# Kernel tuning notes

Hardware: AMD Instinct MI355X
Metric: run time of the kernel (lower is better)

The kernel has to match this reference:

```python
import jax, jax.numpy as jnp
import numpy as np

B, N, C = 16, 576, 1024
H, HD = 16, 64          # num_heads, head_dim
LMAX = 1024             # KV cache capacity
CUR = 256               # pre-existing cur_kv_len
HID = 4096              # mlp hidden
PREFIX = 64             # fixed prefix length from source
EPS = 1e-5


def _ln(x, w, b):
    m = x.mean(-1, keepdims=True)
    v = ((x - m) ** 2).mean(-1, keepdims=True)
    return (x - m) * jax.lax.rsqrt(v + EPS) * w + b


def setup_inputs() -> dict:
    key = jax.random.key(0)
    ks = jax.random.split(key, 8)
    s = 0.02
    return {
        "x": jax.random.normal(ks[0], (B, N, C), jnp.float32),
        "cache_k": jax.random.normal(ks[1], (B, H, LMAX, HD), jnp.float32),
        "cache_v": jax.random.normal(ks[2], (B, H, LMAX, HD), jnp.float32),
        "qkv_w": jax.random.normal(ks[3], (C, 3 * C), jnp.float32) * s,
        "qkv_b": jnp.zeros((3 * C,), jnp.float32),
        "proj_w": jax.random.normal(ks[4], (C, C), jnp.float32) * s,
        "proj_b": jnp.zeros((C,), jnp.float32),
        "norm1_w": jnp.ones((C,), jnp.float32),
        "norm1_b": jnp.zeros((C,), jnp.float32),
        "norm2_w": jnp.ones((C,), jnp.float32),
        "norm2_b": jnp.zeros((C,), jnp.float32),
        "fc1_w": jax.random.normal(ks[5], (C, HID), jnp.float32) * s,
        "fc1_b": jnp.zeros((HID,), jnp.float32),
        "fc2_w": jax.random.normal(ks[6], (HID, C), jnp.float32) * s,
        "fc2_b": jnp.zeros((C,), jnp.float32),
        "cur_kv_len": CUR,
    }


def reference(x, cache_k, cache_v, qkv_w, qkv_b, proj_w, proj_b,
              norm1_w, norm1_b, norm2_w, norm2_b,
              fc1_w, fc1_b, fc2_w, fc2_b, cur_kv_len):
    b, n, c = x.shape
    hd = c // H
    scale = hd ** -0.5

    # ---- attention branch (lazy_mar, not force-fresh) ----
    h = _ln(x, norm1_w, norm1_b)
    qkv = (h @ qkv_w + qkv_b).reshape(b, n, 3, H, hd).transpose(2, 0, 3, 1, 4)
    q, k, v = qkv[0], qkv[1], qkv[2]          # [B,H,N,hd]

    L = cur_kv_len                            # python int -> static slices
    app = n - PREFIX
    # scatter new keys/values into the cache: prefix at [0:64], lazy region appended
    ck = cache_k.at[:, :, PREFIX + L:PREFIX + L + app, :].set(k[:, :, PREFIX:, :])
    ck = ck.at[:, :, :PREFIX, :].set(k[:, :, :PREFIX, :])
    cv = cache_v.at[:, :, PREFIX + L:PREFIX + L + app, :].set(v[:, :, PREFIX:, :])
    cv = cv.at[:, :, :PREFIX, :].set(v[:, :, :PREFIX, :])

    avail = L + n                             # (L + app) + 64
    attn = jax.nn.softmax(
        jnp.einsum('bhqd,bhkd->bhqk', q * scale, ck[:, :, :avail, :]), axis=-1)
    o = jnp.einsum('bhqk,bhkd->bhqd', attn, cv[:, :, :avail, :])
    o = o.transpose(0, 2, 1, 3).reshape(b, n, c)
    x = x + (o @ proj_w + proj_b)

    # ---- MLP branch ----
    h2 = _ln(x, norm2_w, norm2_b)
    mlp = jax.nn.gelu(h2 @ fc1_w + fc1_b, approximate=False) @ fc2_w + fc2_b
    return x + mlp
```

## Files before the change

### kernel.cpp

```cpp
#include <hip/hip_runtime.h>

#define Bb 16
#define Nn_ 576
#define Cc 1024
#define Hh 16
#define HD 64
#define HID 4096
#define AVAIL 832
#define ROWS (Bb*Nn_)

typedef __bf16 bf16x8 __attribute__((ext_vector_type(8)));
typedef float f32x4 __attribute__((ext_vector_type(4)));

__device__ __forceinline__ unsigned short f2bf(float f) {
  unsigned u = __float_as_uint(f);
  u += 0x7FFF + ((u >> 16) & 1);
  return (unsigned short)(u >> 16);
}

__device__ __forceinline__ void glds16(const void* g, void* l) {
  __builtin_amdgcn_global_load_lds(
      (const __attribute__((address_space(1))) void*)g,
      (__attribute__((address_space(3))) void*)l, 16, 0, 0);
}

__device__ __forceinline__ bf16x8 ds_read128(const void* p) {
  bf16x8 r;
  asm volatile("ds_read_b128 %0, %1"
               : "=v"(r)
               : "v"((const __attribute__((address_space(3))) char*)p));
  return r;
}

#define BARR() asm volatile("s_barrier" ::: "memory")
#define VMCNT4() asm volatile("s_waitcnt vmcnt(4)" ::: "memory")
#define VMCNT0() asm volatile("s_waitcnt vmcnt(0)" ::: "memory")
#define LGKM0() asm volatile("s_waitcnt lgkmcnt(0)" ::: "memory")
#define LGKM8() asm volatile("s_waitcnt lgkmcnt(8)" ::: "memory")
#define SCHEDB() __builtin_amdgcn_sched_barrier(0)

__global__ void wtrans_k(const float* __restrict__ in, unsigned short* __restrict__ out,
                         int K, int N) {
  __shared__ float tile[32][33];
  int k0 = blockIdx.x * 32, n0 = blockIdx.y * 32;
  int tx = threadIdx.x, ty = threadIdx.y;
#pragma unroll
  for (int i = 0; i < 4; i++)
    tile[ty + i * 8][tx] = in[(size_t)(k0 + ty + i * 8) * N + n0 + tx];
  __syncthreads();
#pragma unroll
  for (int i = 0; i < 4; i++)
    out[(size_t)(n0 + ty + i * 8) * K + k0 + tx] = f2bf(tile[tx][ty + i * 8]);
}

__global__ void ln_k(const float* __restrict__ x, const float* __restrict__ w,
                     const float* __restrict__ bi, unsigned short* __restrict__ out) {
  int row = blockIdx.x;
  int t = threadIdx.x;
  float4 v = ((const float4*)(x + (size_t)row * Cc))[t];
  float s = v.x + v.y + v.z + v.w;
  float s2 = v.x * v.x + v.y * v.y + v.z * v.z + v.w * v.w;
#pragma unroll
  for (int off = 1; off < 64; off <<= 1) { s += __shfl_xor(s, off); s2 += __shfl_xor(s2, off); }
  __shared__ float red[8];
  int wid = t >> 6, lane = t & 63;
  if (lane == 0) { red[wid] = s; red[4 + wid] = s2; }
  __syncthreads();
  s = red[0] + red[1] + red[2] + red[3];
  s2 = red[4] + red[5] + red[6] + red[7];
  float mean = s * (1.0f / Cc);
  float var = s2 * (1.0f / Cc) - mean * mean;
  float rstd = rsqrtf(var + 1e-5f);
  float4 wv = ((const float4*)w)[t];
  float4 bv = ((const float4*)bi)[t];
  ushort4 ov;
  ov.x = f2bf((v.x - mean) * rstd * wv.x + bv.x);
  ov.y = f2bf((v.y - mean) * rstd * wv.y + bv.y);
  ov.z = f2bf((v.z - mean) * rstd * wv.z + bv.z);
  ov.w = f2bf((v.w - mean) * rstd * wv.w + bv.w);
  *(ushort4*)(out + (size_t)row * Cc + t * 4) = ov;
}

template <int EPI>
__global__ __launch_bounds__(512, 2) void gemm8_k(
    const unsigned short* __restrict__ A, const unsigned short* __restrict__ Bt,
    const float* __restrict__ bias, const float* __restrict__ resid,
    void* __restrict__ outv, int N, int K) {
  extern __shared__ __align__(16) char smem[];
  char* A0buf = smem;
  char* B0buf = smem + 32768;
  char* A1buf = smem + 65536;
  char* B1buf = smem + 98304;

  const int tid = threadIdx.x, lane = tid & 63, wid = tid >> 6;
  const int wr = wid >> 2, wc = wid & 3;
  const int l15 = lane & 15, l4 = lane >> 4;

  const int nwg = gridDim.x * gridDim.y;
  const int bid = blockIdx.y * gridDim.x + blockIdx.x;
  const int swz = (bid & 7) * (nwg >> 3) + (bid >> 3);
  const int m0 = (swz % gridDim.x) * 256, n0 = (swz / gridDim.x) * 256;

  const int KT = K >> 6;
  const size_t K2 = (size_t)K * 2;

  const int toff = (tid >> 3) * (int)K2 + ((((tid & 7) ^ ((tid >> 3) & 7)) << 4));
  const char* As0 = (const char*)A + (size_t)m0 * K2 + toff;
  const char* As1 = As0 + 128 * K2;
  const char* Bs0 = (const char*)Bt + (size_t)n0 * K2 + toff;
  const char* Bs1 = Bs0 + 128 * K2;
  const size_t l64 = 64 * K2;
  const int dst = tid * 16;

  const int s0 = ((l4 ^ (l15 & 7)) << 4);
  const int rbA = (wr * 128 + l15) * 128;
  const int rbB = (wc * 64 + l15) * 128;

  f32x4 acc[2][2][4][2] = {};
  bf16x8 a0[4][2], a1[4][2], bb0[2][2], bb1[2][2];

#define STAGE(srcH, ktb, ldsT, half)                        \
  do {                                                      \
    const char* _g = (srcH) + (size_t)(ktb);                \
    glds16(_g, (ldsT) + (half) * 16384 + dst);              \
    glds16(_g + l64, (ldsT) + (half) * 16384 + 8192 + dst); \
  } while (0)

#define RD_A(dA, CA, mh)                                                           \
  _Pragma("unroll") for (int mi = 0; mi < 4; ++mi)                                 \
  _Pragma("unroll") for (int ks = 0; ks < 2; ++ks)                                 \
    dA[mi][ks] = ds_read128((CA) + rbA + (mh) * 8192 + mi * 2048 + (s0 ^ (ks << 6)));

#define RD_B(dB, CB, nh)                                                           \
  _Pragma("unroll") for (int ni = 0; ni < 2; ++ni)                                 \
  _Pragma("unroll") for (int ks = 0; ks < 2; ++ks)                                 \
    dB[ni][ks] = ds_read128((CB) + rbB + (nh) * 4096 + ni * 2048 + (s0 ^ (ks << 6)));

#define MF(mh, nh, av, bv)                                                         \
  _Pragma("unroll") for (int mi = 0; mi < 4; ++mi)                                 \
  _Pragma("unroll") for (int ni = 0; ni < 2; ++ni)                                 \
  _Pragma("unroll") for (int ks = 0; ks < 2; ++ks)                                 \
    acc[mh][nh][mi][ni] = __builtin_amdgcn_mfma_f32_16x16x32_bf16(                 \
        av[mi][ks], bv[ni][ks], acc[mh][nh][mi][ni], 0, 0, 0);

#define TILE(CA, CB, OA, OB, t)                                       \
  do {                                                                \
    const size_t kt1 = (size_t)((t) + 1) * 128;                       \
    const size_t kt2 = (size_t)((t) + 2) * 128;                       \
                         \
    RD_A(a0, CA, 0); RD_B(bb0, CB, 0);                                \
    STAGE(Bs1, kt1, OB, 1);                                           \
    LGKM8();                                                          \
    BARR(); LGKM0(); SCHEDB();                                        \
    __builtin_amdgcn_s_setprio(1); MF(0, 0, a0, bb0);                 \
    __builtin_amdgcn_s_setprio(0); BARR();                            \
                         \
    RD_B(bb1, CB, 1);                                                 \
    STAGE(As1, kt1, OA, 1);                                           \
    BARR(); LGKM0(); SCHEDB();                                        \
    __builtin_amdgcn_s_setprio(1); MF(0, 1, a0, bb1);                 \
    __builtin_amdgcn_s_setprio(0); BARR();                            \
     \
    RD_A(a1, CA, 1);                                                  \
    STAGE(Bs0, kt2, CB, 0);                                           \
    BARR(); LGKM0(); SCHEDB();                                        \
    __builtin_amdgcn_s_setprio(1); MF(1, 0, a1, bb0);                 \
    __builtin_amdgcn_s_setprio(0); BARR();                            \
         \
    STAGE(As0, kt2, CA, 0);                                           \
    VMCNT4(); BARR();                                                 \
    __builtin_amdgcn_s_setprio(1); MF(1, 1, a1, bb1);                 \
    __builtin_amdgcn_s_setprio(0); BARR();                            \
  } while (0)

#define TILE_T1(CA, CB, OA, OB, t)                                    \
  do {                                                                \
    const size_t kt1 = (size_t)((t) + 1) * 128;                       \
    RD_A(a0, CA, 0); RD_B(bb0, CB, 0);                                \
    STAGE(Bs1, kt1, OB, 1);                                           \
    LGKM8();                                                          \
    BARR(); LGKM0(); SCHEDB();                                        \
    __builtin_amdgcn_s_setprio(1); MF(0, 0, a0, bb0);                 \
    __builtin_amdgcn_s_setprio(0); BARR();                            \
    RD_B(bb1, CB, 1);                                                 \
    STAGE(As1, kt1, OA, 1);                                           \
    BARR(); LGKM0(); SCHEDB();                                        \
    __builtin_amdgcn_s_setprio(1); MF(0, 1, a0, bb1);                 \
    __builtin_amdgcn_s_setprio(0); BARR();                            \
    RD_A(a1, CA, 1);                                                  \
    BARR(); LGKM0(); SCHEDB();                                        \
    __builtin_amdgcn_s_setprio(1); MF(1, 0, a1, bb0);                 \
    __builtin_amdgcn_s_setprio(0); BARR();                            \
    VMCNT0(); BARR();                                                 \
    __builtin_amdgcn_s_setprio(1); MF(1, 1, a1, bb1);                 \
    __builtin_amdgcn_s_setprio(0); BARR();                            \
  } while (0)

#define TILE_T2(CA, CB)                                               \
  do {                                                                \
    RD_A(a0, CA, 0); RD_B(bb0, CB, 0);                                \
    RD_B(bb1, CB, 1); RD_A(a1, CA, 1);                                \
    LGKM0(); SCHEDB();                                                \
    MF(0, 0, a0, bb0); MF(0, 1, a0, bb1);                             \
    MF(1, 0, a1, bb0); MF(1, 1, a1, bb1);                             \
  } while (0)

  STAGE(As0, 0, A0buf, 0);
  STAGE(Bs0, 0, B0buf, 0);
  STAGE(As1, 0, A0buf, 1);
  STAGE(Bs1, 0, B0buf, 1);
  STAGE(Bs0, 128, B1buf, 0);
  STAGE(As0, 128, A1buf, 0);
  VMCNT4();
  BARR();

#pragma unroll 1
  for (int t = 0; t + 3 < KT; t += 2) {
    TILE(A0buf, B0buf, A1buf, B1buf, t);
    TILE(A1buf, B1buf, A0buf, B0buf, t + 1);
  }
  TILE_T1(A0buf, B0buf, A1buf, B1buf, KT - 2);
  TILE_T2(A1buf, B1buf);

  BARR();
  {
    float* eb = (float*)(smem + wid * 16384);
    const int gc0 = n0 + wc * 64;
    const f32x4 bv4 = *(const f32x4*)&bias[gc0 + l15 * 4];
#pragma unroll
    for (int mh = 0; mh < 2; mh++) {
#pragma unroll
      for (int mi = 0; mi < 4; mi++) {
#pragma unroll
        for (int nh = 0; nh < 2; nh++)
#pragma unroll
          for (int ni = 0; ni < 2; ni++)
#pragma unroll
            for (int j = 0; j < 4; j++)
              eb[(l4 * 4 + j) * 68 + nh * 32 + ni * 16 + l15] = acc[mh][nh][mi][ni][j];
        int gr0 = m0 + wr * 128 + mh * 64 + mi * 16;
#pragma unroll
        for (int k = 0; k < 4; k++) {
          int r = k * 4 + l4;
          f32x4 v = *(const f32x4*)&eb[r * 68 + l15 * 4];
          v += bv4;
          size_t base = (size_t)(gr0 + r) * N + gc0 + l15 * 4;
          if (EPI == 1) {
#pragma unroll
            for (int q = 0; q < 4; q++)
              v[q] = 0.5f * v[q] * (1.0f + erff(v[q] * 0.70710678118f));
          }
          if (EPI == 2) {
            f32x4 rv = *(const f32x4*)&resid[base];
            *(f32x4*)((float*)outv + base) = v + rv;
          } else {
            ushort4 o4;
            o4.x = f2bf(v[0]); o4.y = f2bf(v[1]); o4.z = f2bf(v[2]); o4.w = f2bf(v[3]);
            *(ushort4*)((unsigned short*)outv + base) = o4;
          }
        }
      }
    }
  }
#undef TILE_T2
#undef TILE_T1
#undef TILE
#undef MF
#undef RD_B
#undef RD_A
#undef STAGE
}

__global__ void gatherk_k(const unsigned short* __restrict__ qkv,
                          const float* __restrict__ cache_k,
                          unsigned short* __restrict__ Kg) {
  int bh = blockIdx.y, b = bh >> 4, h = bh & 15;
  int p = blockIdx.x * 4 + (threadIdx.x >> 6);
  int d = threadIdx.x & 63;
  unsigned short val;
  if (p < 64)
    val = qkv[((size_t)(b * Nn_ + p)) * 3072 + 1024 + h * 64 + d];
  else if (p < 320)
    val = f2bf(cache_k[(((size_t)b * Hh + h) * 1024 + p) * 64 + d]);
  else
    val = qkv[((size_t)(b * Nn_ + p - 256)) * 3072 + 1024 + h * 64 + d];
  Kg[(((size_t)bh) * AVAIL + p) * 64 + d] = val;
}

__global__ void gathervt_k(const unsigned short* __restrict__ qkv,
                           const float* __restrict__ cache_v,
                           unsigned short* __restrict__ Vt) {
  __shared__ float tile[32][33];
  int bh = blockIdx.z, b = bh >> 4, h = bh & 15;
  int p0 = blockIdx.x * 32, d0 = blockIdx.y * 32;
  int tx = threadIdx.x, ty = threadIdx.y;
#pragma unroll
  for (int i = 0; i < 4; i++) {
    int p = p0 + ty + i * 8, d = d0 + tx;
    float v;
    if (p < 64)
      v = __uint_as_float((unsigned)qkv[((size_t)(b * Nn_ + p)) * 3072 + 2048 + h * 64 + d] << 16);
    else if (p < 320)
      v = cache_v[(((size_t)b * Hh + h) * 1024 + p) * 64 + d];
    else
      v = __uint_as_float((unsigned)qkv[((size_t)(b * Nn_ + p - 256)) * 3072 + 2048 + h * 64 + d] << 16);
    tile[ty + i * 8][tx] = v;
  }
  __syncthreads();
#pragma unroll
  for (int i = 0; i < 4; i++)
    Vt[(((size_t)bh) * 64 + d0 + ty + i * 8) * AVAIL + p0 + tx] = f2bf(tile[tx][ty + i * 8]);
}

__global__ __launch_bounds__(256) void attn_k(
    const unsigned short* __restrict__ qkv, const unsigned short* __restrict__ Kg,
    const unsigned short* __restrict__ Vt, unsigned short* __restrict__ o) {
  __shared__ __attribute__((aligned(16))) unsigned short Qs[64 * 64];
  __shared__ __attribute__((aligned(16))) unsigned short Ks[64 * 64];
  __shared__ __attribute__((aligned(16))) unsigned short Vs[64 * 64];
  __shared__ __attribute__((aligned(16))) unsigned short Ps[4][16 * 64];

  const int tid = threadIdx.x;
  const int lane = tid & 63;
  const int w = tid >> 6;
  const int qt = blockIdx.x;
  const int bh = blockIdx.y, b = bh >> 4, h = bh & 15;
  const float scale = 0.125f;

  {
    int r = tid >> 3;
    int cb = (tid & 7) << 4;
    const char* qb = (const char*)qkv;
    glds16(qb + ((size_t)(b * Nn_ + qt * 64 + r) * 3072 + h * 64) * 2 + cb, (char*)Qs + tid * 16);
    glds16(qb + ((size_t)(b * Nn_ + qt * 64 + 32 + r) * 3072 + h * 64) * 2 + cb,
           (char*)Qs + 4096 + tid * 16);
  }

  float m_run[4], l_run[4];
  f32x4 oacc[4] = {};
#pragma unroll
  for (int j = 0; j < 4; j++) { m_run[j] = -1e30f; l_run[j] = 0.f; }

  const char* kbase = (const char*)(Kg + (size_t)bh * AVAIL * 64);
  const char* vbase = (const char*)(Vt + (size_t)bh * 64 * AVAIL);

  for (int c = 0; c < 13; c++) {
    __syncthreads();
    glds16(kbase + (size_t)c * 8192 + tid * 16, (char*)Ks + tid * 16);
    glds16(kbase + (size_t)c * 8192 + 4096 + tid * 16, (char*)Ks + 4096 + tid * 16);
    {
      int r = tid >> 3;
      int cb = (tid & 7) << 4;
      glds16(vbase + (size_t)r * (AVAIL * 2) + c * 128 + cb, (char*)Vs + tid * 16);
      glds16(vbase + (size_t)(r + 32) * (AVAIL * 2) + c * 128 + cb, (char*)Vs + 4096 + tid * 16);
    }
    asm volatile("s_waitcnt vmcnt(0)" ::: "memory");
    __syncthreads();

    bf16x8 qf[2];
#pragma unroll
    for (int t = 0; t < 2; t++)
      qf[t] = *(const bf16x8*)&Qs[(w * 16 + (lane & 15)) * 64 + t * 32 + (lane >> 4) * 8];
    f32x4 s[4] = {};
#pragma unroll
    for (int nt = 0; nt < 4; nt++) {
#pragma unroll
      for (int t = 0; t < 2; t++) {
        bf16x8 kf = *(const bf16x8*)&Ks[(nt * 16 + (lane & 15)) * 64 + t * 32 + (lane >> 4) * 8];
        s[nt] = __builtin_amdgcn_mfma_f32_16x16x32_bf16(qf[t], kf, s[nt], 0, 0, 0);
      }
    }

    float p[4][4];
#pragma unroll
    for (int j = 0; j < 4; j++) {
      float mx = fmaxf(fmaxf(s[0][j], s[1][j]), fmaxf(s[2][j], s[3][j])) * scale;
#pragma unroll
      for (int off = 1; off < 16; off <<= 1) mx = fmaxf(mx, __shfl_xor(mx, off));
      float m_new = fmaxf(m_run[j], mx);
      float alpha = __expf(m_run[j] - m_new);
      float sum = 0.f;
#pragma unroll
      for (int nt = 0; nt < 4; nt++) {
        p[nt][j] = __expf(s[nt][j] * scale - m_new);
        sum += p[nt][j];
      }
#pragma unroll
      for (int off = 1; off < 16; off <<= 1) sum += __shfl_xor(sum, off);
      l_run[j] = l_run[j] * alpha + sum;
      m_run[j] = m_new;
#pragma unroll
      for (int nt2 = 0; nt2 < 4; nt2++) oacc[nt2][j] *= alpha;
    }

#pragma unroll
    for (int nt = 0; nt < 4; nt++)
#pragma unroll
      for (int j = 0; j < 4; j++)
        Ps[w][((lane >> 4) * 4 + j) * 64 + nt * 16 + (lane & 15)] = f2bf(p[nt][j]);

    bf16x8 pa[2];
#pragma unroll
    for (int t = 0; t < 2; t++)
      pa[t] = *(const bf16x8*)&Ps[w][(lane & 15) * 64 + t * 32 + (lane >> 4) * 8];
#pragma unroll
    for (int nt2 = 0; nt2 < 4; nt2++) {
#pragma unroll
      for (int t = 0; t < 2; t++) {
        bf16x8 vf = *(const bf16x8*)&Vs[(nt2 * 16 + (lane & 15)) * 64 + t * 32 + (lane >> 4) * 8];
        oacc[nt2] = __builtin_amdgcn_mfma_f32_16x16x32_bf16(pa[t], vf, oacc[nt2], 0, 0, 0);
      }
    }
  }

#pragma unroll
  for (int nt2 = 0; nt2 < 4; nt2++) {
#pragma unroll
    for (int j = 0; j < 4; j++) {
      int q = qt * 64 + w * 16 + (lane >> 4) * 4 + j;
      float v = oacc[nt2][j] / l_run[j];
      o[((size_t)(b * Nn_ + q)) * Cc + h * 64 + nt2 * 16 + (lane & 15)] = f2bf(v);
    }
  }
}

extern "C" void kernel_launch(void* const* d_in, const int* in_sizes, int n_in,
                              void* d_out, int out_size, void* d_ws, size_t ws_size,
                              hipStream_t stream) {
  const float* x = (const float*)d_in[0];
  const float* cache_k = (const float*)d_in[1];
  const float* cache_v = (const float*)d_in[2];
  const float* qkv_w = (const float*)d_in[3];
  const float* qkv_b = (const float*)d_in[4];
  const float* proj_w = (const float*)d_in[5];
  const float* proj_b = (const float*)d_in[6];
  const float* n1w = (const float*)d_in[7];
  const float* n1b = (const float*)d_in[8];
  const float* n2w = (const float*)d_in[9];
  const float* n2b = (const float*)d_in[10];
  const float* fc1w = (const float*)d_in[11];
  const float* fc1b = (const float*)d_in[12];
  const float* fc2w = (const float*)d_in[13];
  const float* fc2b = (const float*)d_in[14];

  char* ws = (char*)d_ws;
  unsigned short* wq_t = (unsigned short*)(ws + 0);
  unsigned short* wp_t = (unsigned short*)(ws + 6291456);
  unsigned short* w1_t = (unsigned short*)(ws + 8388608);
  unsigned short* w2_t = (unsigned short*)(ws + 16777216);
  float* x2           = (float*)(ws + 25165824);
  unsigned short* obuf = (unsigned short*)(ws + 62914560);
  unsigned short* hbuf = (unsigned short*)(ws + 81788928);
  unsigned short* vt   = (unsigned short*)(ws + 100663296);
  unsigned short* qkvb = (unsigned short*)(ws + 127926272);
  unsigned short* kg   = (unsigned short*)(ws + 184549376);
  unsigned short* midb = qkvb;

  hipFuncSetAttribute((const void*)&gemm8_k<0>, hipFuncAttributeMaxDynamicSharedMemorySize, 131072);
  hipFuncSetAttribute((const void*)&gemm8_k<1>, hipFuncAttributeMaxDynamicSharedMemorySize, 131072);
  hipFuncSetAttribute((const void*)&gemm8_k<2>, hipFuncAttributeMaxDynamicSharedMemorySize, 131072);

  dim3 b328(32, 8);
  wtrans_k<<<dim3(32, 96), b328, 0, stream>>>(qkv_w, wq_t, 1024, 3072);
  wtrans_k<<<dim3(32, 32), b328, 0, stream>>>(proj_w, wp_t, 1024, 1024);
  wtrans_k<<<dim3(32, 128), b328, 0, stream>>>(fc1w, w1_t, 1024, 4096);
  wtrans_k<<<dim3(128, 32), b328, 0, stream>>>(fc2w, w2_t, 4096, 1024);

  ln_k<<<ROWS, 256, 0, stream>>>(x, n1w, n1b, hbuf);
  gemm8_k<0><<<dim3(36, 12), 512, 131072, stream>>>(hbuf, wq_t, qkv_b, nullptr, qkvb, 3072, 1024);

  gatherk_k<<<dim3(208, 256), 256, 0, stream>>>(qkvb, cache_k, kg);
  gathervt_k<<<dim3(26, 2, 256), b328, 0, stream>>>(qkvb, cache_v, vt);
  attn_k<<<dim3(9, 256), 256, 0, stream>>>(qkvb, kg, vt, obuf);

  gemm8_k<2><<<dim3(36, 4), 512, 131072, stream>>>(obuf, wp_t, proj_b, x, x2, 1024, 1024);
  ln_k<<<ROWS, 256, 0, stream>>>(x2, n2w, n2b, hbuf);
  gemm8_k<1><<<dim3(36, 16), 512, 131072, stream>>>(hbuf, w1_t, fc1b, nullptr, midb, 4096, 1024);
  gemm8_k<2><<<dim3(36, 4), 512, 131072, stream>>>(midb, w2_t, fc2b, x2, (float*)d_out, 1024, 4096);
}
```

Baseline: 655.7 us.

## Split-K the N=1024 GEMMs with atomic epilogue and double-buffer attention KV

The proj and fc2 GEMMs, which launch only 144 workgroups, now split K in two along a new grid z dimension. Their results are accumulated with float atomicAdd into an output pre-filled by a new initout kernel holding residual plus bias. This targets under-occupancy on the device's many CUs, at the cost of atomic traffic, two extra elementwise passes and nondeterministic summation order. The attention kernel also double-buffers the K/V tiles so the next chunk loads during compute, and loads Q fragments once outside the loop. The block-index swizzle and the LGKM8 wait in the GEMM are removed as well.

```diff
diff --git a/kernel.cpp b/kernel.cpp
--- a/kernel.cpp
+++ b/kernel.cpp
@@ -36,7 +36,6 @@
 #define VMCNT4() asm volatile("s_waitcnt vmcnt(4)" ::: "memory")
 #define VMCNT0() asm volatile("s_waitcnt vmcnt(0)" ::: "memory")
 #define LGKM0() asm volatile("s_waitcnt lgkmcnt(0)" ::: "memory")
-#define LGKM8() asm volatile("s_waitcnt lgkmcnt(8)" ::: "memory")
 #define SCHEDB() __builtin_amdgcn_sched_barrier(0)
 
 __global__ void wtrans_k(const float* __restrict__ in, unsigned short* __restrict__ out,
@@ -81,11 +80,20 @@
   *(ushort4*)(out + (size_t)row * Cc + t * 4) = ov;
 }
 
+__global__ void initout_k(const float* __restrict__ resid, const float* __restrict__ bias,
+                          float* __restrict__ out) {
+  int row = blockIdx.x, t = threadIdx.x;
+  float4 r = ((const float4*)(resid + (size_t)row * Cc))[t];
+  float4 bv = ((const float4*)bias)[t];
+  r.x += bv.x; r.y += bv.y; r.z += bv.z; r.w += bv.w;
+  ((float4*)(out + (size_t)row * Cc))[t] = r;
+}
+
 template <int EPI>
 __global__ __launch_bounds__(512, 2) void gemm8_k(
     const unsigned short* __restrict__ A, const unsigned short* __restrict__ Bt,
     const float* __restrict__ bias, const float* __restrict__ resid,
-    void* __restrict__ outv, int N, int K) {
+    void* __restrict__ outv, int N, int K, int ksplit) {
   extern __shared__ __align__(16) char smem[];
   char* A0buf = smem;
   char* B0buf = smem + 32768;
@@ -95,19 +103,15 @@
   const int tid = threadIdx.x, lane = tid & 63, wid = tid >> 6;
   const int wr = wid >> 2, wc = wid & 3;
   const int l15 = lane & 15, l4 = lane >> 4;
-
-  const int nwg = gridDim.x * gridDim.y;
-  const int bid = blockIdx.y * gridDim.x + blockIdx.x;
-  const int swz = (bid & 7) * (nwg >> 3) + (bid >> 3);
-  const int m0 = (swz % gridDim.x) * 256, n0 = (swz / gridDim.x) * 256;
-
-  const int KT = K >> 6;
+  const int m0 = blockIdx.x * 256, n0 = blockIdx.y * 256;
+  const int KT = ksplit >> 6;
   const size_t K2 = (size_t)K * 2;
+  const size_t kb2 = (size_t)blockIdx.z * ksplit * 2;
 
   const int toff = (tid >> 3) * (int)K2 + ((((tid & 7) ^ ((tid >> 3) & 7)) << 4));
-  const char* As0 = (const char*)A + (size_t)m0 * K2 + toff;
+  const char* As0 = (const char*)A + (size_t)m0 * K2 + toff + kb2;
   const char* As1 = As0 + 128 * K2;
-  const char* Bs0 = (const char*)Bt + (size_t)n0 * K2 + toff;
+  const char* Bs0 = (const char*)Bt + (size_t)n0 * K2 + toff + kb2;
   const char* Bs1 = Bs0 + 128 * K2;
   const size_t l64 = 64 * K2;
   const int dst = tid * 16;
@@ -147,26 +151,21 @@
   do {                                                                \
     const size_t kt1 = (size_t)((t) + 1) * 128;                       \
     const size_t kt2 = (size_t)((t) + 2) * 128;                       \
-                         \
     RD_A(a0, CA, 0); RD_B(bb0, CB, 0);                                \
     STAGE(Bs1, kt1, OB, 1);                                           \
-    LGKM8();                                                          \
     BARR(); LGKM0(); SCHEDB();                                        \
     __builtin_amdgcn_s_setprio(1); MF(0, 0, a0, bb0);                 \
     __builtin_amdgcn_s_setprio(0); BARR();                            \
-                         \
     RD_B(bb1, CB, 1);                                                 \
     STAGE(As1, kt1, OA, 1);                                           \
     BARR(); LGKM0(); SCHEDB();                                        \
     __builtin_amdgcn_s_setprio(1); MF(0, 1, a0, bb1);                 \
     __builtin_amdgcn_s_setprio(0); BARR();                            \
-     \
     RD_A(a1, CA, 1);                                                  \
     STAGE(Bs0, kt2, CB, 0);                                           \
     BARR(); LGKM0(); SCHEDB();                                        \
     __builtin_amdgcn_s_setprio(1); MF(1, 0, a1, bb0);                 \
     __builtin_amdgcn_s_setprio(0); BARR();                            \
-         \
     STAGE(As0, kt2, CA, 0);                                           \
     VMCNT4(); BARR();                                                 \
     __builtin_amdgcn_s_setprio(1); MF(1, 1, a1, bb1);                 \
@@ -178,7 +177,6 @@
     const size_t kt1 = (size_t)((t) + 1) * 128;                       \
     RD_A(a0, CA, 0); RD_B(bb0, CB, 0);                                \
     STAGE(Bs1, kt1, OB, 1);                                           \
-    LGKM8();                                                          \
     BARR(); LGKM0(); SCHEDB();                                        \
     __builtin_amdgcn_s_setprio(1); MF(0, 0, a0, bb0);                 \
     __builtin_amdgcn_s_setprio(0); BARR();                            \
@@ -226,7 +224,8 @@
   {
     float* eb = (float*)(smem + wid * 16384);
     const int gc0 = n0 + wc * 64;
-    const f32x4 bv4 = *(const f32x4*)&bias[gc0 + l15 * 4];
+    f32x4 bv4 = {0.f, 0.f, 0.f, 0.f};
+    if (EPI != 3) bv4 = *(const f32x4*)&bias[gc0 + l15 * 4];
 #pragma unroll
     for (int mh = 0; mh < 2; mh++) {
 #pragma unroll
@@ -250,7 +249,11 @@
             for (int q = 0; q < 4; q++)
               v[q] = 0.5f * v[q] * (1.0f + erff(v[q] * 0.70710678118f));
           }
-          if (EPI == 2) {
+          if (EPI == 3) {
+            float* op = (float*)outv + base;
+#pragma unroll
+            for (int q = 0; q < 4; q++) atomicAdd(&op[q], v[q]);
+          } else if (EPI == 2) {
             f32x4 rv = *(const f32x4*)&resid[base];
             *(f32x4*)((float*)outv + base) = v + rv;
           } else {
@@ -316,8 +319,8 @@
     const unsigned short* __restrict__ qkv, const unsigned short* __restrict__ Kg,
     const unsigned short* __restrict__ Vt, unsigned short* __restrict__ o) {
   __shared__ __attribute__((aligned(16))) unsigned short Qs[64 * 64];
-  __shared__ __attribute__((aligned(16))) unsigned short Ks[64 * 64];
-  __shared__ __attribute__((aligned(16))) unsigned short Vs[64 * 64];
+  __shared__ __attribute__((aligned(16))) unsigned short Ks[2][64 * 64];
+  __shared__ __attribute__((aligned(16))) unsigned short Vs[2][64 * 64];
   __shared__ __attribute__((aligned(16))) unsigned short Ps[4][16 * 64];
 
   const int tid = threadIdx.x;
@@ -327,46 +330,54 @@
   const int bh = blockIdx.y, b = bh >> 4, h = bh & 15;
   const float scale = 0.125f;
 
+  const char* kbase = (const char*)(Kg + (size_t)bh * AVAIL * 64);
+  const char* vbase = (const char*)(Vt + (size_t)bh * 64 * AVAIL);
+  const int vr = tid >> 3;
+  const int vcb = (tid & 7) << 4;
+
+#define STAGE_KV(c, buf)                                                          \
+  do {                                                                            \
+    glds16(kbase + (size_t)(c) * 8192 + tid * 16, (char*)Ks[buf] + tid * 16);     \
+    glds16(kbase + (size_t)(c) * 8192 + 4096 + tid * 16,                          \
+           (char*)Ks[buf] + 4096 + tid * 16);                                     \
+    glds16(vbase + (size_t)vr * (AVAIL * 2) + (c) * 128 + vcb,                    \
+           (char*)Vs[buf] + tid * 16);                                            \
+    glds16(vbase + (size_t)(vr + 32) * (AVAIL * 2) + (c) * 128 + vcb,             \
+           (char*)Vs[buf] + 4096 + tid * 16);                                     \
+  } while (0)
+
   {
-    int r = tid >> 3;
-    int cb = (tid & 7) << 4;
     const char* qb = (const char*)qkv;
-    glds16(qb + ((size_t)(b * Nn_ + qt * 64 + r) * 3072 + h * 64) * 2 + cb, (char*)Qs + tid * 16);
-    glds16(qb + ((size_t)(b * Nn_ + qt * 64 + 32 + r) * 3072 + h * 64) * 2 + cb,
+    glds16(qb + ((size_t)(b * Nn_ + qt * 64 + vr) * 3072 + h * 64) * 2 + vcb,
+           (char*)Qs + tid * 16);
+    glds16(qb + ((size_t)(b * Nn_ + qt * 64 + 32 + vr) * 3072 + h * 64) * 2 + vcb,
            (char*)Qs + 4096 + tid * 16);
   }
+  STAGE_KV(0, 0);
+  asm volatile("s_waitcnt vmcnt(0)" ::: "memory");
+  __syncthreads();
+
+  bf16x8 qf[2];
+#pragma unroll
+  for (int t = 0; t < 2; t++)
+    qf[t] = *(const bf16x8*)&Qs[(w * 16 + (lane & 15)) * 64 + t * 32 + (lane >> 4) * 8];
 
   float m_run[4], l_run[4];
   f32x4 oacc[4] = {};
 #pragma unroll
   for (int j = 0; j < 4; j++) { m_run[j] = -1e30f; l_run[j] = 0.f; }
 
-  const char* kbase = (const char*)(Kg + (size_t)bh * AVAIL * 64);
-  const char* vbase = (const char*)(Vt + (size_t)bh * 64 * AVAIL);
-
   for (int c = 0; c < 13; c++) {
-    __syncthreads();
-    glds16(kbase + (size_t)c * 8192 + tid * 16, (char*)Ks + tid * 16);
-    glds16(kbase + (size_t)c * 8192 + 4096 + tid * 16, (char*)Ks + 4096 + tid * 16);
-    {
-      int r = tid >> 3;
-      int cb = (tid & 7) << 4;
-      glds16(vbase + (size_t)r * (AVAIL * 2) + c * 128 + cb, (char*)Vs + tid * 16);
-      glds16(vbase + (size_t)(r + 32) * (AVAIL * 2) + c * 128 + cb, (char*)Vs + 4096 + tid * 16);
-    }
-    asm volatile("s_waitcnt vmcnt(0)" ::: "memory");
-    __syncthreads();
-
-    bf16x8 qf[2];
-#pragma unroll
-    for (int t = 0; t < 2; t++)
-      qf[t] = *(const bf16x8*)&Qs[(w * 16 + (lane & 15)) * 64 + t * 32 + (lane >> 4) * 8];
+    const int cur = c & 1;
+    if (c < 12) STAGE_KV(c + 1, cur ^ 1);
+
     f32x4 s[4] = {};
 #pragma unroll
     for (int nt = 0; nt < 4; nt++) {
 #pragma unroll
       for (int t = 0; t < 2; t++) {
-        bf16x8 kf = *(const bf16x8*)&Ks[(nt * 16 + (lane & 15)) * 64 + t * 32 + (lane >> 4) * 8];
+        bf16x8 kf =
+            *(const bf16x8*)&Ks[cur][(nt * 16 + (lane & 15)) * 64 + t * 32 + (lane >> 4) * 8];
         s[nt] = __builtin_amdgcn_mfma_f32_16x16x32_bf16(qf[t], kf, s[nt], 0, 0, 0);
       }
     }
@@ -407,10 +418,12 @@
     for (int nt2 = 0; nt2 < 4; nt2++) {
 #pragma unroll
       for (int t = 0; t < 2; t++) {
-        bf16x8 vf = *(const bf16x8*)&Vs[(nt2 * 16 + (lane & 15)) * 64 + t * 32 + (lane >> 4) * 8];
+        bf16x8 vf =
+            *(const bf16x8*)&Vs[cur][(nt2 * 16 + (lane & 15)) * 64 + t * 32 + (lane >> 4) * 8];
         oacc[nt2] = __builtin_amdgcn_mfma_f32_16x16x32_bf16(pa[t], vf, oacc[nt2], 0, 0, 0);
       }
     }
+    __syncthreads();
   }
 
 #pragma unroll
@@ -422,6 +435,7 @@
       o[((size_t)(b * Nn_ + q)) * Cc + h * 64 + nt2 * 16 + (lane & 15)] = f2bf(v);
     }
   }
+#undef STAGE_KV
 }
 
 extern "C" void kernel_launch(void* const* d_in, const int* in_sizes, int n_in,
@@ -459,6 +473,7 @@
   hipFuncSetAttribute((const void*)&gemm8_k<0>, hipFuncAttributeMaxDynamicSharedMemorySize, 131072);
   hipFuncSetAttribute((const void*)&gemm8_k<1>, hipFuncAttributeMaxDynamicSharedMemorySize, 131072);
   hipFuncSetAttribute((const void*)&gemm8_k<2>, hipFuncAttributeMaxDynamicSharedMemorySize, 131072);
+  hipFuncSetAttribute((const void*)&gemm8_k<3>, hipFuncAttributeMaxDynamicSharedMemorySize, 131072);
 
   dim3 b328(32, 8);
   wtrans_k<<<dim3(32, 96), b328, 0, stream>>>(qkv_w, wq_t, 1024, 3072);
@@ -467,14 +482,22 @@
   wtrans_k<<<dim3(128, 32), b328, 0, stream>>>(fc2w, w2_t, 4096, 1024);
 
   ln_k<<<ROWS, 256, 0, stream>>>(x, n1w, n1b, hbuf);
-  gemm8_k<0><<<dim3(36, 12), 512, 131072, stream>>>(hbuf, wq_t, qkv_b, nullptr, qkvb, 3072, 1024);
+  gemm8_k<0><<<dim3(36, 12), 512, 131072, stream>>>(hbuf, wq_t, qkv_b, nullptr, qkvb,
+                                                    3072, 1024, 1024);
 
   gatherk_k<<<dim3(208, 256), 256, 0, stream>>>(qkvb, cache_k, kg);
   gathervt_k<<<dim3(26, 2, 256), b328, 0, stream>>>(qkvb, cache_v, vt);
   attn_k<<<dim3(9, 256), 256, 0, stream>>>(qkvb, kg, vt, obuf);
 
-  gemm8_k<2><<<dim3(36, 4), 512, 131072, stream>>>(obuf, wp_t, proj_b, x, x2, 1024, 1024);
+  initout_k<<<ROWS, 256, 0, stream>>>(x, proj_b, x2);
+  gemm8_k<3><<<dim3(36, 4, 2), 512, 131072, stream>>>(obuf, wp_t, nullptr, nullptr, x2,
+                                                      1024, 1024, 512);
+
   ln_k<<<ROWS, 256, 0, stream>>>(x2, n2w, n2b, hbuf);
-  gemm8_k<1><<<dim3(36, 16), 512, 131072, stream>>>(hbuf, w1_t, fc1b, nullptr, midb, 4096, 1024);
-  gemm8_k<2><<<dim3(36, 4), 512, 131072, stream>>>(midb, w2_t, fc2b, x2, (float*)d_out, 1024, 4096);
-}
+  gemm8_k<1><<<dim3(36, 16), 512, 131072, stream>>>(hbuf, w1_t, fc1b, nullptr, midb,
+                                                    4096, 1024, 1024);
+
+  initout_k<<<ROWS, 256, 0, stream>>>(x2, fc2b, (float*)d_out);
+  gemm8_k<3><<<dim3(36, 4, 2), 512, 131072, stream>>>(midb, w2_t, nullptr, nullptr,
+                                                      (float*)d_out, 1024, 4096, 2048);
+}
```

Measured after the change: 1.139 ms. +73.8%, slower.
